# Performance work log

Hardware: AMD Instinct MI355X
Metric: run time of the kernel (lower is better)

The kernel has to match this reference:

```python
import jax, jax.numpy as jnp
from jax import lax
import numpy as np

B, H, W = 8, 352, 1216
CLIPVARIANCE = 5.0   # init kwarg
MAXRANGE = 32        # init kwarg

# 1-pixel shifts with zero padding. out[...,m,n] = x at the shifted location.
def s_pos_w(x):  # out[..., n] = x[..., n-1]
    return jnp.pad(x[..., :, :-1], ((0, 0), (0, 0), (0, 0), (1, 0)))

def s_neg_w(x):  # out[..., n] = x[..., n+1]
    return jnp.pad(x[..., :, 1:], ((0, 0), (0, 0), (0, 0), (0, 1)))

def s_pos_h(x):  # out[..., m, :] = x[..., m-1, :]
    return jnp.pad(x[..., :-1, :], ((0, 0), (0, 0), (1, 0), (0, 0)))

def s_neg_h(x):  # out[..., m, :] = x[..., m+1, :]
    return jnp.pad(x[..., 1:, :], ((0, 0), (0, 0), (0, 1), (0, 0)))


def _dir_accumulate(shift, logstep, depthin, maskf, var_d):
    """Scan outward up to MAXRANGE steps in one direction, accumulating
    confidence weights exp(-min(var, clip)) and variance-weighted depth
    hypotheses depth[src] * exp(integrated log-gradient along the path).
    Paths break at the first unmasked pixel (valid is a running product)."""
    z = jnp.zeros_like(depthin)

    def body(carry, _):
        valid, c, dsh, vsh, aw, awd = carry
        valid = shift(valid * maskf)          # path contiguity
        c = logstep(c)                         # integrated log-depth ratio
        dsh = shift(dsh)                       # source-pixel depth
        vsh = shift(vsh)                       # source-pixel variance
        w = jnp.exp(-jnp.minimum(vsh, CLIPVARIANCE)) * valid
        aw = aw + w
        awd = awd + w * jnp.exp(c) * dsh
        return (valid, c, dsh, vsh, aw, awd), None

    init = (jnp.ones_like(depthin), z, depthin, var_d, z, z)
    (_, _, _, _, aw, awd), _ = lax.scan(body, init, None, length=MAXRANGE)
    return aw, awd


def crf_lateralre(pred_log, mask, variance, depthin):
    """One 4-direction variance-weighted CRF integration pass."""
    maskf = mask.astype(depthin.dtype)
    plog_h = pred_log[:, 0:1]  # log d[m,n+1] - log d[m,n]
    plog_v = pred_log[:, 1:2]  # log d[m+1,n] - log d[m,n]

    dirs = [
        (s_pos_w, lambda c: s_pos_w(c + plog_h), variance[:, 0:1]),  # from left
        (s_neg_w, lambda c: s_neg_w(c) - plog_h, variance[:, 1:2]),  # from right
        (s_pos_h, lambda c: s_pos_h(c + plog_v), variance[:, 2:3]),  # from above
        (s_neg_h, lambda c: s_neg_h(c) - plog_v, variance[:, 3:4]),  # from below
    ]

    tot_w = jnp.zeros_like(depthin)
    tot_wd = jnp.zeros_like(depthin)
    for shift, logstep, var_d in dirs:
        aw, awd = _dir_accumulate(shift, logstep, depthin, maskf, var_d)
        tot_w = tot_w + aw
        tot_wd = tot_wd + awd

    lateralre = jnp.where(tot_w > 0, tot_wd / jnp.maximum(tot_w, 1e-12), 0.0)
    return lateralre * maskf


def setup_inputs() -> dict:
    key = jax.random.key(0)
    k1, k2, k3, k4 = jax.random.split(key, 4)
    pred_log = jax.random.normal(k1, (B, 2, H, W), jnp.float32) * 0.05
    mask = (jax.random.uniform(k2, (B, 1, H, W)) < 0.9).astype(jnp.int32)
    variance = jax.random.uniform(k3, (B, 4, H, W), jnp.float32) * 8.0
    depthin = jax.random.uniform(k4, (B, 1, H, W), jnp.float32) * 10.0 + 1.0
    lam = jnp.array([0.2], jnp.float32)
    return {"pred_log": pred_log, "mask": mask, "variance": variance,
            "depthin": depthin, "lam": lam, "times": 1}


def reference(pred_log, mask, variance, depthin, lam, times):
    depthout = depthin
    for _ in range(times):
        lateralre = crf_lateralre(pred_log, mask, variance, depthout)
        sel = (lateralre > 0).astype(depthin.dtype)
        depthout = (1 - sel) * depthin + sel * (depthin * (1 - lam) + lateralre * lam)
    return depthout
```

## Files before the change

kernel.cpp:

```cpp
#include <hip/hip_runtime.h>
#include <stdint.h>

#define HH 352
#define WW 1216
#define HW (HH*WW)
#define BB 8
#define CLIPV 5.0f
#define MAXR 32

#define VR 44
#define NBAND (HH/VR)
#define PFD 8
#define TOT (VR + MAXR)
#define RING 32

template<int DIR>
__device__ __forceinline__ void vert_scan(
    const int* __restrict__ m, const float* __restrict__ plog_v,
    const float* __restrict__ vp, const float* __restrict__ d,
    const int w, const int h0, const int lane,
    float2 (&obuf)[VR][64])
{
    const int hs   = DIR ? (h0 + VR - 1 + MAXR) : (h0 - MAXR);
    const int step = DIR ? -1 : 1;

    float rq_q[RING], rq_w[RING];
    int   r_mi[PFD];
    float r_pl[PFD], r_vv[PFD], r_dd[PFD];

    #pragma unroll
    for (int p = 0; p < PFD; ++p) {
        int hp = hs + p * step;
        int hc = min(max(hp, 0), HH-1);
        int idx = hc * WW + w;
        r_mi[p] = m[idx];
        r_pl[p] = plog_v[idx];
        r_vv[p] = vp[idx];
        r_dd[p] = d[idx];
    }

    float Q = 0.f, W = 0.f, EG = 1.f;
    int last_inv = hs - step;

    #pragma unroll
    for (int it = 0; it < TOT; ++it) {
        const int h  = hs + it * step;
        const int sl = it % PFD;

        int   mi  = ((unsigned)h < (unsigned)HH) ? r_mi[sl] : 0;
        float pl  = r_pl[sl];
        float vvx = r_vv[sl];
        float dd  = r_dd[sl];

        if (it + PFD < TOT) {
            int hp = h + PFD * step;
            int hc = min(max(hp, 0), HH-1);
            int idx = hc * WW + w;
            r_mi[sl] = m[idx];
            r_pl[sl] = plog_v[idx];
            r_vv[sl] = vp[idx];
            r_dd[sl] = d[idx];
        }

        bool  res = (mi == 0);
        float g   = __expf(pl);
        float wt  = __expf(-fminf(vvx, CLIPV));
        float q, outw, outq;
        if constexpr (DIR == 0) {
            outw = W; outq = EG * Q;
            q = wt * dd * __builtin_amdgcn_rcpf(EG);
            Q  = res ? 0.f : (Q + q);
            W  = res ? 0.f : (W + wt);
            EG = res ? 1.f : (EG * g);
        } else {
            float EDh = EG * g;
            outw = W; outq = Q * __builtin_amdgcn_rcpf(EDh);
            q = wt * dd * EDh;
            Q  = res ? 0.f : (Q + q);
            W  = res ? 0.f : (W + wt);
            EG = res ? 1.f : EDh;
        }
        last_inv = res ? h : last_inv;

        if (it >= MAXR) {
            const int r = DIR ? (VR - 1 - (it - MAXR)) : (it - MAXR);
            obuf[r][lane] = make_float2(outw, outq);
            int s_out = h - MAXR * step;
            bool alive = DIR ? (s_out < last_inv) : (s_out > last_inv);
            Q -= alive ? rq_q[it & (RING-1)] : 0.f;
            W -= alive ? rq_w[it & (RING-1)] : 0.f;
        }
        if (it < VR) { rq_q[it & (RING-1)] = q; rq_w[it & (RING-1)] = wt; }
    }
}

__global__ __launch_bounds__(128) void crf_vert(
    const float* __restrict__ pred_log, const int* __restrict__ mask,
    const float* __restrict__ variance, const float* __restrict__ depth,
    float2* __restrict__ vq)
{
    __shared__ float2 obufA[VR][64];
    __shared__ float2 obufB[VR][64];

    const int lane = threadIdx.x & 63;
    const int dir  = threadIdx.x >> 6;
    const int id   = blockIdx.x;
    const int band = id & 7;
    const int seq  = id >> 3;
    const int wc   = seq % 19;
    const int b    = seq / 19;
    const int w    = wc * 64 + lane;

    const float* plog_v = pred_log + ((size_t)b*2 + 1) * HW;
    const int*   m  = mask     + (size_t)b*HW;
    const float* vp = variance + ((size_t)b*4 + (dir ? 3 : 2)) * HW;
    const float* d  = depth    + (size_t)b*HW;

    const int h0 = band * VR;

    if (dir == 0) {
        vert_scan<0>(m, plog_v, vp, d, w, h0, lane, obufA);
    } else {
        vert_scan<1>(m, plog_v, vp, d, w, h0, lane, obufB);
    }

    __syncthreads();
    {
        float2* pvq = vq + (size_t)b*HW;
        const int w0c = wc * 64;
        const int rbeg = dir * (VR/2);
        #pragma unroll
        for (int r2 = 0; r2 < VR/2; ++r2) {
            const int r = rbeg + r2;
            float2 a = obufA[r][lane];
            float2 c = obufB[r][lane];
            pvq[(h0 + r) * WW + w0c + lane] = make_float2(a.x + c.x, a.y + c.y);
        }
    }
}

__global__ __launch_bounds__(256) void crf_horiz(
    const float* __restrict__ pred_log, const int* __restrict__ mask,
    const float* __restrict__ variance, const float* __restrict__ depth,
    const float* __restrict__ lam_p,
    const float2* __restrict__ vq,
    float* __restrict__ out)
{
    __shared__ float sG[WW];
    __shared__ float sH[WW];
    __shared__ float sI[WW];
    __shared__ float sJ[WW];
    __shared__ float sEt[19], sEti[19], sTw0[19], sTq0[19];
    __shared__ unsigned long long sBal[19];

    const int tid  = threadIdx.x;
    const int lane = tid & 63;
    const int wv   = tid >> 6;
    const int i    = blockIdx.x;
    const int h    = (i & 7) * 44 + (i >> 3);
    const int b    = blockIdx.y;

    const float* plrow = pred_log + (size_t)b*2*HW + h*WW;
    const int*   mrow  = mask     + (size_t)b*HW   + h*WW;
    const float* v0row = variance + (size_t)b*4*HW + h*WW;
    const float* v1row = v0row + HW;
    const float* drow  = depth    + (size_t)b*HW   + h*WW;
    const float2* vqrow= vq  + (size_t)b*HW + h*WW;
    float*       orow  = out + (size_t)b*HW + h*WW;

    float l_pAx[5], l_xw0[5], l_xq0[5], l_iw1[5], l_iq1[5], l_m[5], l_d[5];

    #pragma unroll
    for (int r = 0; r < 5; ++r) {
        int c = r*4 + wv;
        if (c < 19) {
            int j = c*64 + lane;
            float pl  = plrow[j];
            int   mi  = mrow[j];
            float dj  = drow[j];
            float wt0 = __expf(-fminf(v0row[j], CLIPV));
            float wt1 = __expf(-fminf(v1row[j], CLIPV));
            float ipA = pl;
            #pragma unroll
            for (int dlt = 1; dlt < 64; dlt <<= 1) {
                float u = __shfl_up(ipA, dlt, 64);
                if (lane >= dlt) ipA += u;
            }
            float pAx = ipA - pl;
            float S   = __shfl(ipA, 63, 64);
            float Einv = __expf(-pAx);
            float q0 = wt0 * dj * Einv;
            float q1 = wt1 * dj * Einv;
            float iw0 = wt0, iq0 = q0, iw1 = wt1, iq1 = q1;
            #pragma unroll
            for (int dlt = 1; dlt < 64; dlt <<= 1) {
                float a = __shfl_up(iw0, dlt, 64);
                float e = __shfl_up(iq0, dlt, 64);
                float f = __shfl_up(iw1, dlt, 64);
                float g = __shfl_up(iq1, dlt, 64);
                if (lane >= dlt) { iw0 += a; iq0 += e; iw1 += f; iq1 += g; }
            }
            sG[j] = iw0 - wt0;
            sH[j] = iq0 - q0;
            sI[j] = iw1;
            sJ[j] = iq1;
            unsigned long long bal = __ballot(mi == 0);
            if (lane == 63) {
                sEt[c]  = __expf(S);
                sEti[c] = __expf(-S);
                sTw0[c] = iw0;
                sTq0[c] = iq0;
            }
            if (lane == 0) sBal[c] = bal;
            l_pAx[r] = pAx; l_xw0[r] = iw0 - wt0; l_xq0[r] = iq0 - q0;
            l_iw1[r] = iw1; l_iq1[r] = iq1;
            l_m[r] = (float)mi; l_d[r] = dj;
        }
    }
    __syncthreads();

    const float lam = lam_p[0];

    #pragma unroll
    for (int r = 0; r < 5; ++r) {
        int c = r*4 + wv;
        if (c < 19) {
            const int c0 = c*64;
            const int j  = c0 + lane;
            float E = __expf(l_pAx[r]);
            unsigned long long balOwn = sBal[c];
            unsigned long long mb = balOwn & ((1ull << lane) - 1ull);
            int lm = mb ? (c0 + 63 - __builtin_clzll(mb)) : -1;
            if (c > 0 && lane < 32) {
                unsigned long long mp = sBal[c-1] & ~((1ull << (lane + 32)) - 1ull);
                if (mp) { int lm2 = c0 - 64 + 63 - __builtin_clzll(mp); lm = max(lm, lm2); }
            }
            int a0 = max(j - MAXR, lm + 1);
            float W0, Q0;
            if (a0 >= c0) {
                W0 = l_xw0[r] - sG[a0];
                Q0 = E * (l_xq0[r] - sH[a0]);
            } else {
                W0 = l_xw0[r] + (sTw0[c-1] - sG[a0]);
                Q0 = E * l_xq0[r] + E * sEt[c-1] * (sTq0[c-1] - sH[a0]);
            }
            int nm = 1 << 30;
            if (lane < 63) {
                unsigned long long nb = balOwn >> (lane + 1);
                if (nb) nm = j + 1 + __builtin_ctzll(nb);
            }
            if (c < 18 && lane >= 32) {
                unsigned long long nn = sBal[c+1] & ((1ull << (lane - 31)) - 1ull);
                if (nn) nm = min(nm, c0 + 64 + (int)__builtin_ctzll(nn));
            }
            int b1 = min(j + MAXR, nm - 1);
            b1 = min(b1, WW - 1);
            int endin = min(b1, c0 + 63);
            float W1 = 0.f, Q1 = 0.f;
            if (endin > j) {
                W1 = sI[endin] - l_iw1[r];
                Q1 = E * (sJ[endin] - l_iq1[r]);
            }
            if (b1 > c0 + 63) {
                W1 += sI[b1];
                Q1 += E * sEti[c] * sJ[b1];
            }
            float2 vt = vqrow[j];
            float totw  = W0 + W1 + vt.x;
            float totwd = Q0 + Q1 + vt.y;
            float lat = (totw > 0.f) ? (totwd / fmaxf(totw, 1e-12f)) : 0.f;
            lat *= l_m[r];
            float dj = l_d[r];
            orow[j] = (lat > 0.f) ? (dj * (1.f - lam) + lat * lam) : dj;
        }
    }
}

#define BWF 256
#define PADF 32
#define LWF (BWF + 2*PADF)

__global__ __launch_bounds__(256) void crf_fallback(
    const float* __restrict__ pred_log, const int* __restrict__ mask,
    const float* __restrict__ variance, const float* __restrict__ depth,
    const float* __restrict__ lam_p, float* __restrict__ out)
{
    __shared__ float s_m[LWF], s_wt0[LWF], s_wt1[LWF], s_gh[LWF], s_ghi[LWF], s_d[LWF];
    const int t  = threadIdx.x;
    const int i  = blockIdx.x;
    const int h  = (i & 7) * 44 + (i >> 3);
    const int w0 = blockIdx.y * BWF;
    const int b  = blockIdx.z;
    const float* plog_h = pred_log + (size_t)b * 2 * HW;
    const float* plog_v = plog_h + HW;
    const int*   m      = mask   + (size_t)b * HW;
    const float* v0     = variance + (size_t)b * 4 * HW;
    const float* v1     = v0 + HW;
    const float* v2     = v0 + 2 * HW;
    const float* v3     = v0 + 3 * HW;
    const float* d      = depth + (size_t)b * HW;
    for (int j = t; j < LWF; j += BWF) {
        int gw = w0 - PADF + j;
        float mf=0.f, wt0=0.f, wt1=0.f, gh=1.f, ghi=1.f, dd=0.f;
        if (gw >= 0 && gw < WW) {
            int idx = h * WW + gw;
            mf = (float)m[idx];
            float pl = plog_h[idx];
            gh = __expf(pl); ghi = __expf(-pl);
            wt0 = __expf(-fminf(v0[idx], CLIPV));
            wt1 = __expf(-fminf(v1[idx], CLIPV));
            dd = d[idx];
        }
        s_m[j]=mf; s_wt0[j]=wt0; s_wt1[j]=wt1; s_gh[j]=gh; s_ghi[j]=ghi; s_d[j]=dd;
    }
    __syncthreads();
    const int w = w0 + t;
    if (w >= WW) return;
    const int c = t + PADF;
    float totw = 0.f, totwd = 0.f;
    { float e=1.f, valid=1.f;
      #pragma unroll 8
      for (int k=1;k<=MAXR;++k){int s=c-k; valid*=s_m[s]; e*=s_gh[s];
        float wgt=s_wt0[s]*valid; totw+=wgt; totwd+=wgt*e*s_d[s];} }
    { float e=1.f, valid=1.f;
      #pragma unroll 8
      for (int k=1;k<=MAXR;++k){int s=c+k; e*=s_ghi[s-1]; valid*=s_m[s];
        float wgt=s_wt1[s]*valid; totw+=wgt; totwd+=wgt*e*s_d[s];} }
    { const int kup=min(MAXR,h); float e=1.f, valid=1.f;
      #pragma unroll 4
      for (int k=1;k<=kup;++k){int idx=(h-k)*WW+w; valid*=(float)m[idx];
        e*=__expf(plog_v[idx]); float wgt=__expf(-fminf(v2[idx],CLIPV))*valid;
        totw+=wgt; totwd+=wgt*e*d[idx];} }
    { const int kdn=min(MAXR,HH-1-h); float e=1.f, valid=1.f;
      #pragma unroll 4
      for (int k=1;k<=kdn;++k){int idx=(h+k)*WW+w; e*=__expf(-plog_v[idx-WW]);
        valid*=(float)m[idx]; float wgt=__expf(-fminf(v3[idx],CLIPV))*valid;
        totw+=wgt; totwd+=wgt*e*d[idx];} }
    const int base = h * WW + w;
    float lat = (totw > 0.f) ? (totwd / fmaxf(totw, 1e-12f)) : 0.f;
    lat *= s_m[c];
    float lam = lam_p[0];
    float di  = s_d[c];
    out[(size_t)b * HW + base] = (lat > 0.f) ? (di * (1.f - lam) + lat * lam) : di;
}

extern "C" void kernel_launch(void* const* d_in, const int* in_sizes, int n_in,
                              void* d_out, int out_size, void* d_ws, size_t ws_size,
                              hipStream_t stream) {
    const float* pred_log = (const float*)d_in[0];
    const int*   mask     = (const int*)  d_in[1];
    const float* variance = (const float*)d_in[2];
    const float* depthin  = (const float*)d_in[3];
    const float* lam      = (const float*)d_in[4];
    float* out = (float*)d_out;

    const size_t need = (size_t)BB * HW * sizeof(float2);
    if (ws_size >= need) {
        float2* vq = (float2*)d_ws;
        dim3 vgrid(19 * NBAND * BB, 1, 1);
        hipLaunchKernelGGL(crf_vert, vgrid, dim3(128), 0, stream,
                           pred_log, mask, variance, depthin, vq);
        dim3 hgrid(HH, BB);
        hipLaunchKernelGGL(crf_horiz, hgrid, dim3(256), 0, stream,
                           pred_log, mask, variance, depthin, lam, vq, out);
    } else {
        dim3 fgrid(HH, (WW + BWF - 1) / BWF, BB);
        hipLaunchKernelGGL(crf_fallback, fgrid, dim3(BWF), 0, stream,
                           pred_log, mask, variance, depthin, lam, out);
    }
}
```

Baseline: 178.3 us.

## Process two pixels per lane in horizontal CRF pass with 128-wide chunks

The horizontal pass now has each lane handle two adjacent pixels. Rows are split into 10 chunks of 128 instead of 19 chunks of 64. Loads and stores use float2/float4 vectors, and the wave-level prefix scans run over pair sums, which roughly halves shuffle work per pixel. Mask ballots are split into even and odd bitmaps, so the break-point search becomes more complex and uses more registers. The last chunk is padded past the row end and needs careful bounds clamping.

```diff
diff --git a/kernel.cpp b/kernel.cpp
--- a/kernel.cpp
+++ b/kernel.cpp
@@ -139,6 +139,70 @@
     }
 }
 
+#define NCH 10
+#define CW 128
+
+__device__ __forceinline__ float2 horiz_combine(
+    int c, int c0, int p, int j, float E,
+    float sGj, float sHj, float iw1j, float iq1j,
+    const float* sG, const float* sH, const float* sI, const float* sJ,
+    const float* sEt, const float* sEti, const float* sTw0, const float* sTq0,
+    const unsigned long long* sBalE, const unsigned long long* sBalO)
+{
+    const int L = p >> 1, e = p & 1;
+    const unsigned long long balE = sBalE[c], balO = sBalO[c];
+    unsigned long long belowE = e ? (balE & ((2ULL << L) - 1ULL))
+                                  : (balE & ((1ULL << L) - 1ULL));
+    unsigned long long belowO = balO & ((1ULL << L) - 1ULL);
+    int lm = -1;
+    if (belowE) lm = c0 + 2 * (63 - __builtin_clzll(belowE));
+    if (belowO) lm = max(lm, c0 + 2 * (63 - __builtin_clzll(belowO)) + 1);
+    if (c > 0 && p < MAXR) {
+        const int T  = CW - MAXR + p;
+        const int KE = (T + 1) >> 1;
+        const int KO = T >> 1;
+        unsigned long long mpE = (KE < 64) ? (sBalE[c-1] & ~((1ULL << KE) - 1ULL)) : 0ULL;
+        unsigned long long mpO = sBalO[c-1] & ~((1ULL << KO) - 1ULL);
+        if (mpE) lm = max(lm, c0 - CW + 2 * (63 - __builtin_clzll(mpE)));
+        if (mpO) lm = max(lm, c0 - CW + 2 * (63 - __builtin_clzll(mpO)) + 1);
+    }
+    int a0 = max(j - MAXR, lm + 1);
+    float W0, Q0;
+    if (a0 >= c0) {
+        W0 = sGj - sG[a0];
+        Q0 = E * (sHj - sH[a0]);
+    } else {
+        W0 = sGj + (sTw0[c-1] - sG[a0]);
+        Q0 = E * sHj + E * sEt[c-1] * (sTq0[c-1] - sH[a0]);
+    }
+    int nm = 1 << 30;
+    unsigned long long nbE = balE & ~((2ULL << L) - 1ULL);
+    unsigned long long nbO = e ? (balO & ~((2ULL << L) - 1ULL))
+                               : (balO & ~((1ULL << L) - 1ULL));
+    if (nbE) nm = c0 + 2 * __builtin_ctzll(nbE);
+    if (nbO) nm = min(nm, c0 + 2 * __builtin_ctzll(nbO) + 1);
+    if (c < NCH - 1 && p >= CW - MAXR) {
+        const int T2 = p - (CW - MAXR);
+        unsigned long long nnE = sBalE[c+1] & ((2ULL << (T2 >> 1)) - 1ULL);
+        unsigned long long nnO = (T2 >= 1) ? (sBalO[c+1] & ((2ULL << ((T2 - 1) >> 1)) - 1ULL)) : 0ULL;
+        if (nnE) nm = min(nm, c0 + CW + 2 * __builtin_ctzll(nnE));
+        if (nnO) nm = min(nm, c0 + CW + 2 * __builtin_ctzll(nnO) + 1);
+    }
+    int b1 = min(j + MAXR, nm - 1);
+    b1 = min(b1, WW - 1);
+    int endin = min(b1, c0 + CW - 1);
+    float W1 = 0.f, Q1 = 0.f;
+    if (endin > j) {
+        W1 = sI[endin] - iw1j;
+        Q1 = E * (sJ[endin] - iq1j);
+    }
+    if (b1 > c0 + CW - 1) {
+        W1 += sI[b1];
+        Q1 += E * sEti[c] * sJ[b1];
+    }
+    return make_float2(W0 + W1, Q0 + Q1);
+}
+
 __global__ __launch_bounds__(256) void crf_horiz(
     const float* __restrict__ pred_log, const int* __restrict__ mask,
     const float* __restrict__ variance, const float* __restrict__ depth,
@@ -146,12 +210,12 @@
     const float2* __restrict__ vq,
     float* __restrict__ out)
 {
-    __shared__ float sG[WW];
-    __shared__ float sH[WW];
-    __shared__ float sI[WW];
-    __shared__ float sJ[WW];
-    __shared__ float sEt[19], sEti[19], sTw0[19], sTq0[19];
-    __shared__ unsigned long long sBal[19];
+    __shared__ float sG[NCH*CW];
+    __shared__ float sH[NCH*CW];
+    __shared__ float sI[NCH*CW];
+    __shared__ float sJ[NCH*CW];
+    __shared__ float sEt[NCH], sEti[NCH], sTw0[NCH], sTq0[NCH];
+    __shared__ unsigned long long sBalE[NCH], sBalO[NCH];
 
     const int tid  = threadIdx.x;
     const int lane = tid & 63;
@@ -168,53 +232,85 @@
     const float2* vqrow= vq  + (size_t)b*HW + h*WW;
     float*       orow  = out + (size_t)b*HW + h*WW;
 
-    float l_pAx[5], l_xw0[5], l_xq0[5], l_iw1[5], l_iq1[5], l_m[5], l_d[5];
+    float l_pAx0[3], l_pAx1[3], l_d0[3], l_d1[3], l_mi0[3], l_mi1[3];
+    float l_vw0[3], l_vq0[3], l_vw1[3], l_vq1[3];
+    float l_sG0[3], l_sG1[3], l_sH0[3], l_sH1[3];
+    float l_w1i0[3], l_w1i1[3], l_q1i0[3], l_q1i1[3];
 
     #pragma unroll
-    for (int r = 0; r < 5; ++r) {
+    for (int r = 0; r < 3; ++r) {
         int c = r*4 + wv;
-        if (c < 19) {
-            int j = c*64 + lane;
-            float pl  = plrow[j];
-            int   mi  = mrow[j];
-            float dj  = drow[j];
-            float wt0 = __expf(-fminf(v0row[j], CLIPV));
-            float wt1 = __expf(-fminf(v1row[j], CLIPV));
-            float ipA = pl;
+        if (c < NCH) {
+            const int c0 = c*CW;
+            const int p0 = 2*lane;
+            const int j0 = c0 + p0;
+            const int jc = min(j0, WW-2);
+            float2 plv = *reinterpret_cast<const float2*>(&plrow[jc]);
+            int2   miv = *reinterpret_cast<const int2*>(&mrow[jc]);
+            float2 dv  = *reinterpret_cast<const float2*>(&drow[jc]);
+            float2 v0v = *reinterpret_cast<const float2*>(&v0row[jc]);
+            float2 v1v = *reinterpret_cast<const float2*>(&v1row[jc]);
+            float4 vtv = *reinterpret_cast<const float4*>(&vqrow[jc]);
+            const bool valid = (j0 < WW);
+            float pl0 = valid ? plv.x : 0.f;
+            float pl1 = valid ? plv.y : 0.f;
+            int   mi0 = valid ? miv.x : 0;
+            int   mi1 = valid ? miv.y : 0;
+            float d0  = dv.x, d1 = dv.y;
+            float wt00 = valid ? __expf(-fminf(v0v.x, CLIPV)) : 0.f;
+            float wt01 = valid ? __expf(-fminf(v0v.y, CLIPV)) : 0.f;
+            float wt10 = valid ? __expf(-fminf(v1v.x, CLIPV)) : 0.f;
+            float wt11 = valid ? __expf(-fminf(v1v.y, CLIPV)) : 0.f;
+
+            float sp = pl0 + pl1;
+            float ip = sp;
             #pragma unroll
             for (int dlt = 1; dlt < 64; dlt <<= 1) {
-                float u = __shfl_up(ipA, dlt, 64);
-                if (lane >= dlt) ipA += u;
+                float u = __shfl_up(ip, dlt, 64);
+                if (lane >= dlt) ip += u;
             }
-            float pAx = ipA - pl;
-            float S   = __shfl(ipA, 63, 64);
-            float Einv = __expf(-pAx);
-            float q0 = wt0 * dj * Einv;
-            float q1 = wt1 * dj * Einv;
-            float iw0 = wt0, iq0 = q0, iw1 = wt1, iq1 = q1;
+            float pAx0 = ip - sp;
+            float pAx1 = ip - pl1;
+            float S = __shfl(ip, 63, 64);
+            float Ei0 = __expf(-pAx0), Ei1 = __expf(-pAx1);
+            float q00 = wt00*d0*Ei0, q01 = wt01*d1*Ei1;
+            float q10 = wt10*d0*Ei0, q11 = wt11*d1*Ei1;
+
+            float aw0 = wt00+wt01, aq0 = q00+q01, aw1 = wt10+wt11, aq1 = q10+q11;
+            float Iw0 = aw0, Iq0 = aq0, Iw1 = aw1, Iq1 = aq1;
             #pragma unroll
             for (int dlt = 1; dlt < 64; dlt <<= 1) {
-                float a = __shfl_up(iw0, dlt, 64);
-                float e = __shfl_up(iq0, dlt, 64);
-                float f = __shfl_up(iw1, dlt, 64);
-                float g = __shfl_up(iq1, dlt, 64);
-                if (lane >= dlt) { iw0 += a; iq0 += e; iw1 += f; iq1 += g; }
+                float ua = __shfl_up(Iw0, dlt, 64);
+                float ub = __shfl_up(Iq0, dlt, 64);
+                float uc = __shfl_up(Iw1, dlt, 64);
+                float ud = __shfl_up(Iq1, dlt, 64);
+                if (lane >= dlt) { Iw0 += ua; Iq0 += ub; Iw1 += uc; Iq1 += ud; }
             }
-            sG[j] = iw0 - wt0;
-            sH[j] = iq0 - q0;
-            sI[j] = iw1;
-            sJ[j] = iq1;
-            unsigned long long bal = __ballot(mi == 0);
+            float sg0 = Iw0 - aw0,  sg1 = Iw0 - wt01;
+            float sh0 = Iq0 - aq0,  sh1 = Iq0 - q01;
+            float si0 = Iw1 - wt11, si1 = Iw1;
+            float sj0 = Iq1 - q11,  sj1 = Iq1;
+            *reinterpret_cast<float2*>(&sG[j0 < NCH*CW ? j0 : 0]) = make_float2(sg0, sg1);
+            *reinterpret_cast<float2*>(&sH[j0 < NCH*CW ? j0 : 0]) = make_float2(sh0, sh1);
+            *reinterpret_cast<float2*>(&sI[j0 < NCH*CW ? j0 : 0]) = make_float2(si0, si1);
+            *reinterpret_cast<float2*>(&sJ[j0 < NCH*CW ? j0 : 0]) = make_float2(sj0, sj1);
+
+            unsigned long long balE = __ballot(mi0 == 0);
+            unsigned long long balO = __ballot(mi1 == 0);
             if (lane == 63) {
                 sEt[c]  = __expf(S);
                 sEti[c] = __expf(-S);
-                sTw0[c] = iw0;
-                sTq0[c] = iq0;
+                sTw0[c] = Iw0;
+                sTq0[c] = Iq0;
             }
-            if (lane == 0) sBal[c] = bal;
-            l_pAx[r] = pAx; l_xw0[r] = iw0 - wt0; l_xq0[r] = iq0 - q0;
-            l_iw1[r] = iw1; l_iq1[r] = iq1;
-            l_m[r] = (float)mi; l_d[r] = dj;
+            if (lane == 0) { sBalE[c] = balE; sBalO[c] = balO; }
+
+            l_pAx0[r] = pAx0; l_pAx1[r] = pAx1;
+            l_d0[r] = d0; l_d1[r] = d1;
+            l_mi0[r] = (float)mi0; l_mi1[r] = (float)mi1;
+            l_vw0[r] = vtv.x; l_vq0[r] = vtv.y; l_vw1[r] = vtv.z; l_vq1[r] = vtv.w;
+            l_sG0[r] = sg0; l_sG1[r] = sg1; l_sH0[r] = sh0; l_sH1[r] = sh1;
+            l_w1i0[r] = si0; l_w1i1[r] = si1; l_q1i0[r] = sj0; l_q1i1[r] = sj1;
         }
     }
     __syncthreads();
@@ -222,56 +318,29 @@
     const float lam = lam_p[0];
 
     #pragma unroll
-    for (int r = 0; r < 5; ++r) {
+    for (int r = 0; r < 3; ++r) {
         int c = r*4 + wv;
-        if (c < 19) {
-            const int c0 = c*64;
-            const int j  = c0 + lane;
-            float E = __expf(l_pAx[r]);
-            unsigned long long balOwn = sBal[c];
-            unsigned long long mb = balOwn & ((1ull << lane) - 1ull);
-            int lm = mb ? (c0 + 63 - __builtin_clzll(mb)) : -1;
-            if (c > 0 && lane < 32) {
-                unsigned long long mp = sBal[c-1] & ~((1ull << (lane + 32)) - 1ull);
-                if (mp) { int lm2 = c0 - 64 + 63 - __builtin_clzll(mp); lm = max(lm, lm2); }
+        if (c < NCH) {
+            const int c0 = c*CW;
+            const int p0 = 2*lane;
+            const int j0 = c0 + p0;
+            if (j0 < WW) {
+                float2 wq0 = horiz_combine(c, c0, p0,   j0,   __expf(l_pAx0[r]),
+                    l_sG0[r], l_sH0[r], l_w1i0[r], l_q1i0[r],
+                    sG, sH, sI, sJ, sEt, sEti, sTw0, sTq0, sBalE, sBalO);
+                float2 wq1 = horiz_combine(c, c0, p0+1, j0+1, __expf(l_pAx1[r]),
+                    l_sG1[r], l_sH1[r], l_w1i1[r], l_q1i1[r],
+                    sG, sH, sI, sJ, sEt, sEti, sTw0, sTq0, sBalE, sBalO);
+                float totw0 = wq0.x + l_vw0[r], totq0 = wq0.y + l_vq0[r];
+                float totw1 = wq1.x + l_vw1[r], totq1 = wq1.y + l_vq1[r];
+                float lat0 = (totw0 > 0.f) ? (totq0 / fmaxf(totw0, 1e-12f)) : 0.f;
+                float lat1 = (totw1 > 0.f) ? (totq1 / fmaxf(totw1, 1e-12f)) : 0.f;
+                lat0 *= l_mi0[r];
+                lat1 *= l_mi1[r];
+                float o0 = (lat0 > 0.f) ? (l_d0[r]*(1.f-lam) + lat0*lam) : l_d0[r];
+                float o1 = (lat1 > 0.f) ? (l_d1[r]*(1.f-lam) + lat1*lam) : l_d1[r];
+                *reinterpret_cast<float2*>(&orow[j0]) = make_float2(o0, o1);
             }
-            int a0 = max(j - MAXR, lm + 1);
-            float W0, Q0;
-            if (a0 >= c0) {
-                W0 = l_xw0[r] - sG[a0];
-                Q0 = E * (l_xq0[r] - sH[a0]);
-            } else {
-                W0 = l_xw0[r] + (sTw0[c-1] - sG[a0]);
-                Q0 = E * l_xq0[r] + E * sEt[c-1] * (sTq0[c-1] - sH[a0]);
-            }
-            int nm = 1 << 30;
-            if (lane < 63) {
-                unsigned long long nb = balOwn >> (lane + 1);
-                if (nb) nm = j + 1 + __builtin_ctzll(nb);
-            }
-            if (c < 18 && lane >= 32) {
-                unsigned long long nn = sBal[c+1] & ((1ull << (lane - 31)) - 1ull);
-                if (nn) nm = min(nm, c0 + 64 + (int)__builtin_ctzll(nn));
-            }
-            int b1 = min(j + MAXR, nm - 1);
-            b1 = min(b1, WW - 1);
-            int endin = min(b1, c0 + 63);
-            float W1 = 0.f, Q1 = 0.f;
-            if (endin > j) {
-                W1 = sI[endin] - l_iw1[r];
-                Q1 = E * (sJ[endin] - l_iq1[r]);
-            }
-            if (b1 > c0 + 63) {
-                W1 += sI[b1];
-                Q1 += E * sEti[c] * sJ[b1];
-            }
-            float2 vt = vqrow[j];
-            float totw  = W0 + W1 + vt.x;
-            float totwd = Q0 + Q1 + vt.y;
-            float lat = (totw > 0.f) ? (totwd / fmaxf(totw, 1e-12f)) : 0.f;
-            lat *= l_m[r];
-            float dj = l_d[r];
-            orow[j] = (lat > 0.f) ? (dj * (1.f - lam) + lat * lam) : dj;
         }
     }
 }
```

Result: no change. 175.0 us (-1.8%).
